# Optimization experiments

Hardware: AMD Instinct MI355X
Metric: run time of the kernel (lower is better)

The kernel has to match this reference:

```python
import jax, jax.numpy as jnp
import numpy as np

B, H, W = 16, 352, 352
EPS = 1e-7

# Directable[TL_table[i]] for i = 0..7: (dx, dy), dx=+1 shifts right, dy=+1 shifts down
# TL_table = [lower_right, down, lower_left, right, left, upper_right, up, upper_left]
SHIFTS = [(1, 1), (0, 1), (-1, 1), (1, 0), (-1, 0), (1, -1), (0, -1), (-1, -1)]


def _shift(x, dx, dy):
    # x: [B,H,W]; zero-padded translation, equivalent to the bmm against the
    # near-identity translation matrices in the original code.
    if dx == 1:
        x = jnp.pad(x, ((0, 0), (0, 0), (1, 0)))[:, :, :-1]
    elif dx == -1:
        x = jnp.pad(x, ((0, 0), (0, 0), (0, 1)))[:, :, 1:]
    if dy == 1:
        x = jnp.pad(x, ((0, 0), (1, 0), (0, 0)))[:, :-1, :]
    elif dy == -1:
        x = jnp.pad(x, ((0, 0), (0, 1), (0, 0)))[:, 1:, :]
    return x


def _bce_sum(p, t):
    p = jnp.clip(p, EPS, 1.0 - EPS)
    return -jnp.sum(t * jnp.log(p) + (1.0 - t) * jnp.log1p(-p))


def setup_inputs() -> dict:
    key = jax.random.key(0)
    k1, k2, k3 = jax.random.split(key, 3)
    c_map = jax.random.normal(k1, (B, 8, H, W), dtype=jnp.float32)
    target = jax.random.uniform(k2, (B, 1, H, W), dtype=jnp.float32)
    con_target = jax.random.randint(k3, (B, 8, H, W), 0, 2, dtype=jnp.int32)
    return {"c_map": c_map, "target": target, "con_target": con_target}


def reference(c_map, target, con_target):
    p = jax.nn.sigmoid(c_map)                      # [B,8,H,W]
    con = con_target.astype(p.dtype)
    sum_conn = jnp.sum(con, axis=1)                # [B,H,W]
    edge = ((sum_conn < 8) & (sum_conn > 0)).astype(p.dtype)

    # Bilateral voting: shifted[:, i] = shift(p[:, 7-i], direction_i)
    shifted = jnp.stack(
        [_shift(p[:, 7 - i], *SHIFTS[i]) for i in range(8)], axis=1
    )                                              # [B,8,H,W]
    vote = p * shifted                             # [B,8,H,W]

    glo_map = jnp.max(vote, axis=1)                # [B,H,W]
    pred_mask_min = jnp.min(vote, axis=1)          # [B,H,W]
    decouple = glo_map * (1.0 - edge) + (1.0 - pred_mask_min) * edge

    de_loss = _bce_sum(decouple[:, None], target)
    conmap_l = _bce_sum(p, con)
    bimap_l = _bce_sum(vote, con)
    return 0.8 * conmap_l + de_loss + 0.2 * bimap_l
```

## Files before the change

kernel.cpp:

```cpp
#include <hip/hip_runtime.h>


#define EPSF 1e-7f

constexpr int B = 16, H = 352, W = 352;
constexpr int HW = H * W;
constexpr int TILE_PX = 2816;
constexpr int TILES = HW / TILE_PX;
constexpr int NBLK = B * TILES;
constexpr int TILE_Q = TILE_PX / 4;
constexpr int HALO = 384;
constexpr int STAGE_PX = TILE_PX + 2 * HALO;
constexpr int STAGE_Q  = STAGE_PX / 4;
constexpr int STAGE_ALL_Q = 8 * STAGE_Q;
constexpr int SITER = STAGE_ALL_Q / 256;

typedef float    f4 __attribute__((ext_vector_type(4)));
typedef int      i4 __attribute__((ext_vector_type(4)));
typedef _Float16 h4 __attribute__((ext_vector_type(4)));

__device__ __forceinline__ float rcpf(float x) { return __builtin_amdgcn_rcpf(x); }

__device__ __forceinline__ f4 sigmoid4(f4 x) {
    f4 r;
    r.x = rcpf(1.0f + __expf(-x.x));
    r.y = rcpf(1.0f + __expf(-x.y));
    r.z = rcpf(1.0f + __expf(-x.z));
    r.w = rcpf(1.0f + __expf(-x.w));
    return r;
}
__device__ __forceinline__ f4 max4(f4 a, f4 b) {
    f4 r; r.x=fmaxf(a.x,b.x); r.y=fmaxf(a.y,b.y); r.z=fmaxf(a.z,b.z); r.w=fmaxf(a.w,b.w); return r;
}
__device__ __forceinline__ f4 min4(f4 a, f4 b) {
    f4 r; r.x=fminf(a.x,b.x); r.y=fminf(a.y,b.y); r.z=fminf(a.z,b.z); r.w=fminf(a.w,b.w); return r;
}
__device__ __forceinline__ f4 sel4(i4 m, f4 a, f4 b) {
    f4 r; r.x=m.x?a.x:b.x; r.y=m.y?a.y:b.y; r.z=m.z?a.z:b.z; r.w=m.w?a.w:b.w; return r;
}
__device__ __forceinline__ f4 cvt4(h4 h) {
    f4 r; r.x=(float)h.x; r.y=(float)h.y; r.z=(float)h.z; r.w=(float)h.w; return r;
}
__device__ __forceinline__ f4 rd4(const _Float16* p) {
    f4 r; r.x=(float)p[0]; r.y=(float)p[1]; r.z=(float)p[2]; r.w=(float)p[3]; return r;
}

__device__ __forceinline__ float finish_pixel(float glo, float pmin, int sc,
                                              float t, float cp, float ba, float bb) {
    const float edge = (sc < 8 && sc > 0) ? 1.0f : 0.0f;
    float dec = glo * (1.0f - edge) + (1.0f - pmin) * edge;
    dec = fminf(fmaxf(dec, EPSF), 1.0f - EPSF);
    const float de = -(t * __logf(dec) + (1.0f - t) * __logf(1.0f - dec));
    return de - 0.8f * __logf(cp) - 0.2f * (__logf(ba) + __logf(bb));
}

__global__ __launch_bounds__(256) void bicon_loss_kernel(
    const float* __restrict__ c_map,
    const float* __restrict__ target,
    const int*   __restrict__ con,
    float* __restrict__ ws)
{
    __shared__ _Float16 Lh[8 * STAGE_PX];
    __shared__ float wsum[4];

    const int blk  = blockIdx.x;
    const int b    = blk / TILES;
    const int tile = blk - b * TILES;
    const int s    = tile * TILE_PX;
    const int s0   = s - HALO;

    const float* __restrict__ cmb = c_map + (size_t)b * 8 * HW;
    const int*   __restrict__ cnb = con   + (size_t)b * 8 * HW;
    const float* __restrict__ tgb = target + (size_t)b * HW;

    #pragma unroll
    for (int k = 0; k < SITER; ++k) {
        const int q   = threadIdx.x + k * 256;
        const int ch  = q / STAGE_Q;
        const int idx = q - ch * STAGE_Q;
        int px = s0 + idx * 4;
        px = px < 0 ? 0 : (px > HW - 4 ? HW - 4 : px);
        const f4 v = *(const f4*)(cmb + ch * HW + px);
        const f4 p = sigmoid4(v);
        h4 hp; hp.x=(_Float16)p.x; hp.y=(_Float16)p.y; hp.z=(_Float16)p.z; hp.w=(_Float16)p.w;
        *(h4*)(&Lh[q * 4]) = hp;
    }
    __syncthreads();

    float part = 0.0f;
    #pragma unroll
    for (int k = 0; k < 3; ++k) {
        const int qi = threadIdx.x + k * 256;
        if (qi < TILE_Q) {
            const int gp  = s + qi * 4;
            const int y   = gp / W;
            const int xq4 = (gp - y * W) >> 2;
            const float lm = (xq4 == 0)         ? 0.0f : 1.0f;
            const float rm = (xq4 == W / 4 - 1) ? 0.0f : 1.0f;
            const float tm = (y == 0)           ? 0.0f : 1.0f;
            const float bm = (y == H - 1)       ? 0.0f : 1.0f;
            const int l0 = qi * 4 + HALO;

            const i4 g0 = *(const i4*)(cnb + 0 * HW + gp);
            const i4 g1 = *(const i4*)(cnb + 1 * HW + gp);
            const i4 g2 = *(const i4*)(cnb + 2 * HW + gp);
            const i4 g3 = *(const i4*)(cnb + 3 * HW + gp);
            const i4 g4 = *(const i4*)(cnb + 4 * HW + gp);
            const i4 g5 = *(const i4*)(cnb + 5 * HW + gp);
            const i4 g6 = *(const i4*)(cnb + 6 * HW + gp);
            const i4 g7 = *(const i4*)(cnb + 7 * HW + gp);
            const f4 t4 = *(const f4*)(tgb + gp);

            const f4 p0 = cvt4(*(const h4*)&Lh[0 * STAGE_PX + l0]);
            const f4 p1 = cvt4(*(const h4*)&Lh[1 * STAGE_PX + l0]);
            const f4 p2 = cvt4(*(const h4*)&Lh[2 * STAGE_PX + l0]);
            const f4 p3 = cvt4(*(const h4*)&Lh[3 * STAGE_PX + l0]);
            const f4 p4 = cvt4(*(const h4*)&Lh[4 * STAGE_PX + l0]);
            const f4 p5 = cvt4(*(const h4*)&Lh[5 * STAGE_PX + l0]);
            const f4 p6 = cvt4(*(const h4*)&Lh[6 * STAGE_PX + l0]);
            const f4 p7 = cvt4(*(const h4*)&Lh[7 * STAGE_PX + l0]);
            const f4 n0 = rd4(&Lh[7 * STAGE_PX + l0 - W - 1]);
            const f4 n1 = cvt4(*(const h4*)&Lh[6 * STAGE_PX + l0 - W]);
            const f4 n2 = rd4(&Lh[5 * STAGE_PX + l0 - W + 1]);
            const f4 n3 = rd4(&Lh[4 * STAGE_PX + l0 - 1]);
            const f4 n4 = rd4(&Lh[3 * STAGE_PX + l0 + 1]);
            const f4 n5 = rd4(&Lh[2 * STAGE_PX + l0 + W - 1]);
            const f4 n6 = cvt4(*(const h4*)&Lh[1 * STAGE_PX + l0 + W]);
            const f4 n7 = rd4(&Lh[0 * STAGE_PX + l0 + W + 1]);

            f4 conprod = {1.f,1.f,1.f,1.f};
            f4 biA     = {1.f,1.f,1.f,1.f};
            f4 biB     = {1.f,1.f,1.f,1.f};
            f4 glo     = {-1e30f,-1e30f,-1e30f,-1e30f};
            f4 pmin    = { 1e30f, 1e30f, 1e30f, 1e30f};

#define DIR(P, G, S, DX, RMASK, BI) {                                         \
            f4 sv = (S);                                                      \
            sv *= (RMASK);                                                    \
            if ((DX) == 1)  sv.x *= lm;                                       \
            if ((DX) == -1) sv.w *= rm;                                       \
            const f4 v = (P) * sv;                                            \
            glo  = max4(glo,  v);                                             \
            pmin = min4(pmin, v);                                             \
            conprod *= sel4((G), (P), 1.0f - (P));                            \
            BI *= sel4((G), max4(v, (f4){EPSF,EPSF,EPSF,EPSF}), 1.0f - v);    \
        }
            DIR(p0, g0, n0,  1, tm,   biA)
            DIR(p1, g1, n1,  0, tm,   biA)
            DIR(p2, g2, n2, -1, tm,   biA)
            DIR(p3, g3, n3,  1, 1.0f, biA)
            DIR(p4, g4, n4, -1, 1.0f, biB)
            DIR(p5, g5, n5,  1, bm,   biB)
            DIR(p6, g6, n6,  0, bm,   biB)
            DIR(p7, g7, n7, -1, bm,   biB)
#undef DIR

            const i4 sc = g0 + g1 + g2 + g3 + g4 + g5 + g6 + g7;
            part += finish_pixel(glo.x, pmin.x, sc.x, t4.x, conprod.x, biA.x, biB.x)
                  + finish_pixel(glo.y, pmin.y, sc.y, t4.y, conprod.y, biA.y, biB.y)
                  + finish_pixel(glo.z, pmin.z, sc.z, t4.z, conprod.z, biA.z, biB.z)
                  + finish_pixel(glo.w, pmin.w, sc.w, t4.w, conprod.w, biA.w, biB.w);
        }
    }

    #pragma unroll
    for (int off = 32; off > 0; off >>= 1)
        part += __shfl_down(part, off, 64);

    const int lane = threadIdx.x & 63;
    const int wid  = threadIdx.x >> 6;
    if (lane == 0) wsum[wid] = part;
    __syncthreads();
    if (threadIdx.x == 0)
        ws[blockIdx.x] = wsum[0] + wsum[1] + wsum[2] + wsum[3];
}

__global__ __launch_bounds__(256) void reduce_partials_kernel(
    const float* __restrict__ ws, float* __restrict__ out)
{
    float s = 0.0f;
    for (int i = threadIdx.x; i < NBLK; i += 256) s += ws[i];
    #pragma unroll
    for (int off = 32; off > 0; off >>= 1)
        s += __shfl_down(s, off, 64);
    __shared__ float wsum[4];
    const int lane = threadIdx.x & 63;
    const int wid  = threadIdx.x >> 6;
    if (lane == 0) wsum[wid] = s;
    __syncthreads();
    if (threadIdx.x == 0) out[0] = wsum[0] + wsum[1] + wsum[2] + wsum[3];
}

extern "C" void kernel_launch(void* const* d_in, const int* in_sizes, int n_in,
                              void* d_out, int out_size, void* d_ws, size_t ws_size,
                              hipStream_t stream) {
    const float* c_map  = (const float*)d_in[0];
    const float* target = (const float*)d_in[1];
    const int*   con    = (const int*)d_in[2];
    float* out = (float*)d_out;
    float* ws  = (float*)d_ws;

    bicon_loss_kernel<<<NBLK, 256, 0, stream>>>(c_map, target, con, ws);
    reduce_partials_kernel<<<1, 256, 0, stream>>>(ws, out);
}
```

Baseline: 150.7 us.

## Stage raw logits via async global_load_lds with smaller tiles, sigmoid at use

Tiles shrink from 2816 to 704 pixels so each thread handles exactly one quad, which gives four times as many blocks. Raw fp32 logits are now copied straight into LDS with the direct global-to-LDS load instruction instead of being converted through registers to fp16. The con and target loads are issued before the barrier so they overlap the staging. Sigmoid is now computed at the point of use, which doubles the exp work per pixel (own value and neighbour), and the halo re-read per block grows sharply relative to the tile size.

```diff
diff --git a/kernel.cpp b/kernel.cpp
--- a/kernel.cpp
+++ b/kernel.cpp
@@ -5,19 +5,17 @@
 
 constexpr int B = 16, H = 352, W = 352;
 constexpr int HW = H * W;
-constexpr int TILE_PX = 2816;
+constexpr int TILE_PX = 704;
 constexpr int TILES = HW / TILE_PX;
 constexpr int NBLK = B * TILES;
 constexpr int TILE_Q = TILE_PX / 4;
-constexpr int HALO = 384;
+constexpr int HALO = 416;
 constexpr int STAGE_PX = TILE_PX + 2 * HALO;
 constexpr int STAGE_Q  = STAGE_PX / 4;
-constexpr int STAGE_ALL_Q = 8 * STAGE_Q;
-constexpr int SITER = STAGE_ALL_Q / 256;
-
-typedef float    f4 __attribute__((ext_vector_type(4)));
-typedef int      i4 __attribute__((ext_vector_type(4)));
-typedef _Float16 h4 __attribute__((ext_vector_type(4)));
+constexpr int SITER = 8 * STAGE_Q / 256;
+
+typedef float f4 __attribute__((ext_vector_type(4)));
+typedef int   i4 __attribute__((ext_vector_type(4)));
 
 __device__ __forceinline__ float rcpf(float x) { return __builtin_amdgcn_rcpf(x); }
 
@@ -38,11 +36,14 @@
 __device__ __forceinline__ f4 sel4(i4 m, f4 a, f4 b) {
     f4 r; r.x=m.x?a.x:b.x; r.y=m.y?a.y:b.y; r.z=m.z?a.z:b.z; r.w=m.w?a.w:b.w; return r;
 }
-__device__ __forceinline__ f4 cvt4(h4 h) {
-    f4 r; r.x=(float)h.x; r.y=(float)h.y; r.z=(float)h.z; r.w=(float)h.w; return r;
-}
-__device__ __forceinline__ f4 rd4(const _Float16* p) {
-    f4 r; r.x=(float)p[0]; r.y=(float)p[1]; r.z=(float)p[2]; r.w=(float)p[3]; return r;
+__device__ __forceinline__ f4 rd4f(const float* p) {
+    f4 r; r.x=p[0]; r.y=p[1]; r.z=p[2]; r.w=p[3]; return r;
+}
+
+__device__ __forceinline__ void load_lds16(const float* g, float* l) {
+    __builtin_amdgcn_global_load_lds(
+        (const __attribute__((address_space(1))) unsigned int*)g,
+        (__attribute__((address_space(3))) unsigned int*)l, 16, 0, 0);
 }
 
 __device__ __forceinline__ float finish_pixel(float glo, float pmin, int sc,
@@ -60,7 +61,7 @@
     const int*   __restrict__ con,
     float* __restrict__ ws)
 {
-    __shared__ _Float16 Lh[8 * STAGE_PX];
+    __shared__ float Lr[8 * STAGE_PX];
     __shared__ float wsum[4];
 
     const int blk  = blockIdx.x;
@@ -75,92 +76,92 @@
 
     #pragma unroll
     for (int k = 0; k < SITER; ++k) {
-        const int q   = threadIdx.x + k * 256;
+        const int q   = k * 256 + threadIdx.x;
         const int ch  = q / STAGE_Q;
         const int idx = q - ch * STAGE_Q;
         int px = s0 + idx * 4;
         px = px < 0 ? 0 : (px > HW - 4 ? HW - 4 : px);
-        const f4 v = *(const f4*)(cmb + ch * HW + px);
-        const f4 p = sigmoid4(v);
-        h4 hp; hp.x=(_Float16)p.x; hp.y=(_Float16)p.y; hp.z=(_Float16)p.z; hp.w=(_Float16)p.w;
-        *(h4*)(&Lh[q * 4]) = hp;
-    }
+        load_lds16(cmb + ch * HW + px, &Lr[q * 4]);
+    }
+
+    const bool act = threadIdx.x < TILE_Q;
+    const int  qi  = threadIdx.x;
+    const int  gp  = s + qi * 4;
+    i4 g0{}, g1{}, g2{}, g3{}, g4{}, g5{}, g6{}, g7{};
+    f4 t4{};
+    if (act) {
+        g0 = *(const i4*)(cnb + 0 * HW + gp);
+        g1 = *(const i4*)(cnb + 1 * HW + gp);
+        g2 = *(const i4*)(cnb + 2 * HW + gp);
+        g3 = *(const i4*)(cnb + 3 * HW + gp);
+        g4 = *(const i4*)(cnb + 4 * HW + gp);
+        g5 = *(const i4*)(cnb + 5 * HW + gp);
+        g6 = *(const i4*)(cnb + 6 * HW + gp);
+        g7 = *(const i4*)(cnb + 7 * HW + gp);
+        t4 = *(const f4*)(tgb + gp);
+    }
+
     __syncthreads();
 
     float part = 0.0f;
-    #pragma unroll
-    for (int k = 0; k < 3; ++k) {
-        const int qi = threadIdx.x + k * 256;
-        if (qi < TILE_Q) {
-            const int gp  = s + qi * 4;
-            const int y   = gp / W;
-            const int xq4 = (gp - y * W) >> 2;
-            const float lm = (xq4 == 0)         ? 0.0f : 1.0f;
-            const float rm = (xq4 == W / 4 - 1) ? 0.0f : 1.0f;
-            const float tm = (y == 0)           ? 0.0f : 1.0f;
-            const float bm = (y == H - 1)       ? 0.0f : 1.0f;
-            const int l0 = qi * 4 + HALO;
-
-            const i4 g0 = *(const i4*)(cnb + 0 * HW + gp);
-            const i4 g1 = *(const i4*)(cnb + 1 * HW + gp);
-            const i4 g2 = *(const i4*)(cnb + 2 * HW + gp);
-            const i4 g3 = *(const i4*)(cnb + 3 * HW + gp);
-            const i4 g4 = *(const i4*)(cnb + 4 * HW + gp);
-            const i4 g5 = *(const i4*)(cnb + 5 * HW + gp);
-            const i4 g6 = *(const i4*)(cnb + 6 * HW + gp);
-            const i4 g7 = *(const i4*)(cnb + 7 * HW + gp);
-            const f4 t4 = *(const f4*)(tgb + gp);
-
-            const f4 p0 = cvt4(*(const h4*)&Lh[0 * STAGE_PX + l0]);
-            const f4 p1 = cvt4(*(const h4*)&Lh[1 * STAGE_PX + l0]);
-            const f4 p2 = cvt4(*(const h4*)&Lh[2 * STAGE_PX + l0]);
-            const f4 p3 = cvt4(*(const h4*)&Lh[3 * STAGE_PX + l0]);
-            const f4 p4 = cvt4(*(const h4*)&Lh[4 * STAGE_PX + l0]);
-            const f4 p5 = cvt4(*(const h4*)&Lh[5 * STAGE_PX + l0]);
-            const f4 p6 = cvt4(*(const h4*)&Lh[6 * STAGE_PX + l0]);
-            const f4 p7 = cvt4(*(const h4*)&Lh[7 * STAGE_PX + l0]);
-            const f4 n0 = rd4(&Lh[7 * STAGE_PX + l0 - W - 1]);
-            const f4 n1 = cvt4(*(const h4*)&Lh[6 * STAGE_PX + l0 - W]);
-            const f4 n2 = rd4(&Lh[5 * STAGE_PX + l0 - W + 1]);
-            const f4 n3 = rd4(&Lh[4 * STAGE_PX + l0 - 1]);
-            const f4 n4 = rd4(&Lh[3 * STAGE_PX + l0 + 1]);
-            const f4 n5 = rd4(&Lh[2 * STAGE_PX + l0 + W - 1]);
-            const f4 n6 = cvt4(*(const h4*)&Lh[1 * STAGE_PX + l0 + W]);
-            const f4 n7 = rd4(&Lh[0 * STAGE_PX + l0 + W + 1]);
-
-            f4 conprod = {1.f,1.f,1.f,1.f};
-            f4 biA     = {1.f,1.f,1.f,1.f};
-            f4 biB     = {1.f,1.f,1.f,1.f};
-            f4 glo     = {-1e30f,-1e30f,-1e30f,-1e30f};
-            f4 pmin    = { 1e30f, 1e30f, 1e30f, 1e30f};
+    if (act) {
+        const int y   = gp / W;
+        const int xq4 = (gp - y * W) >> 2;
+        const float lm = (xq4 == 0)         ? 0.0f : 1.0f;
+        const float rm = (xq4 == W / 4 - 1) ? 0.0f : 1.0f;
+        const float tm = (y == 0)           ? 0.0f : 1.0f;
+        const float bm = (y == H - 1)       ? 0.0f : 1.0f;
+        const int l0 = HALO + qi * 4;
+
+        const f4 p0 = sigmoid4(*(const f4*)&Lr[0 * STAGE_PX + l0]);
+        const f4 p1 = sigmoid4(*(const f4*)&Lr[1 * STAGE_PX + l0]);
+        const f4 p2 = sigmoid4(*(const f4*)&Lr[2 * STAGE_PX + l0]);
+        const f4 p3 = sigmoid4(*(const f4*)&Lr[3 * STAGE_PX + l0]);
+        const f4 p4 = sigmoid4(*(const f4*)&Lr[4 * STAGE_PX + l0]);
+        const f4 p5 = sigmoid4(*(const f4*)&Lr[5 * STAGE_PX + l0]);
+        const f4 p6 = sigmoid4(*(const f4*)&Lr[6 * STAGE_PX + l0]);
+        const f4 p7 = sigmoid4(*(const f4*)&Lr[7 * STAGE_PX + l0]);
+        const f4 n0 = sigmoid4(rd4f(&Lr[7 * STAGE_PX + l0 - W - 1]));
+        const f4 n1 = sigmoid4(*(const f4*)&Lr[6 * STAGE_PX + l0 - W]);
+        const f4 n2 = sigmoid4(rd4f(&Lr[5 * STAGE_PX + l0 - W + 1]));
+        const f4 n3 = sigmoid4(rd4f(&Lr[4 * STAGE_PX + l0 - 1]));
+        const f4 n4 = sigmoid4(rd4f(&Lr[3 * STAGE_PX + l0 + 1]));
+        const f4 n5 = sigmoid4(rd4f(&Lr[2 * STAGE_PX + l0 + W - 1]));
+        const f4 n6 = sigmoid4(*(const f4*)&Lr[1 * STAGE_PX + l0 + W]);
+        const f4 n7 = sigmoid4(rd4f(&Lr[0 * STAGE_PX + l0 + W + 1]));
+
+        f4 conprod = {1.f,1.f,1.f,1.f};
+        f4 biA     = {1.f,1.f,1.f,1.f};
+        f4 biB     = {1.f,1.f,1.f,1.f};
+        f4 glo     = {-1e30f,-1e30f,-1e30f,-1e30f};
+        f4 pmin    = { 1e30f, 1e30f, 1e30f, 1e30f};
 
 #define DIR(P, G, S, DX, RMASK, BI) {                                         \
-            f4 sv = (S);                                                      \
-            sv *= (RMASK);                                                    \
-            if ((DX) == 1)  sv.x *= lm;                                       \
-            if ((DX) == -1) sv.w *= rm;                                       \
-            const f4 v = (P) * sv;                                            \
-            glo  = max4(glo,  v);                                             \
-            pmin = min4(pmin, v);                                             \
-            conprod *= sel4((G), (P), 1.0f - (P));                            \
-            BI *= sel4((G), max4(v, (f4){EPSF,EPSF,EPSF,EPSF}), 1.0f - v);    \
-        }
-            DIR(p0, g0, n0,  1, tm,   biA)
-            DIR(p1, g1, n1,  0, tm,   biA)
-            DIR(p2, g2, n2, -1, tm,   biA)
-            DIR(p3, g3, n3,  1, 1.0f, biA)
-            DIR(p4, g4, n4, -1, 1.0f, biB)
-            DIR(p5, g5, n5,  1, bm,   biB)
-            DIR(p6, g6, n6,  0, bm,   biB)
-            DIR(p7, g7, n7, -1, bm,   biB)
+        f4 sv = (S);                                                          \
+        sv *= (RMASK);                                                        \
+        if ((DX) == 1)  sv.x *= lm;                                           \
+        if ((DX) == -1) sv.w *= rm;                                           \
+        const f4 v = (P) * sv;                                                \
+        glo  = max4(glo,  v);                                                 \
+        pmin = min4(pmin, v);                                                 \
+        conprod *= sel4((G), (P), 1.0f - (P));                                \
+        BI *= sel4((G), max4(v, (f4){EPSF,EPSF,EPSF,EPSF}), 1.0f - v);        \
+    }
+        DIR(p0, g0, n0,  1, tm,   biA)
+        DIR(p1, g1, n1,  0, tm,   biA)
+        DIR(p2, g2, n2, -1, tm,   biA)
+        DIR(p3, g3, n3,  1, 1.0f, biA)
+        DIR(p4, g4, n4, -1, 1.0f, biB)
+        DIR(p5, g5, n5,  1, bm,   biB)
+        DIR(p6, g6, n6,  0, bm,   biB)
+        DIR(p7, g7, n7, -1, bm,   biB)
 #undef DIR
 
-            const i4 sc = g0 + g1 + g2 + g3 + g4 + g5 + g6 + g7;
-            part += finish_pixel(glo.x, pmin.x, sc.x, t4.x, conprod.x, biA.x, biB.x)
-                  + finish_pixel(glo.y, pmin.y, sc.y, t4.y, conprod.y, biA.y, biB.y)
-                  + finish_pixel(glo.z, pmin.z, sc.z, t4.z, conprod.z, biA.z, biB.z)
-                  + finish_pixel(glo.w, pmin.w, sc.w, t4.w, conprod.w, biA.w, biB.w);
-        }
+        const i4 sc = g0 + g1 + g2 + g3 + g4 + g5 + g6 + g7;
+        part = finish_pixel(glo.x, pmin.x, sc.x, t4.x, conprod.x, biA.x, biB.x)
+             + finish_pixel(glo.y, pmin.y, sc.y, t4.y, conprod.y, biA.y, biB.y)
+             + finish_pixel(glo.z, pmin.z, sc.z, t4.z, conprod.z, biA.z, biB.z)
+             + finish_pixel(glo.w, pmin.w, sc.w, t4.w, conprod.w, biA.w, biB.w);
     }
 
     #pragma unroll
```

Measured after the change: 154.7 us. 2.7% more time.
